# Optimization experiments

Hardware: AMD Instinct MI355X
Metric: run time of the kernel (lower is better)

Reference implementation:

```python
import jax, jax.numpy as jnp
import numpy as np
import math

VOCAB = 390
D = 512
D_INNER = 2048
H = 8
DH = D // H
L = 6
MAX_SEQ = 1024
BATCH = 4
OUT = 2
PAD = 0
EPS = 1e-6


def sinusoid(max_seq, d):
    pos = np.arange(max_seq, dtype=np.float64)[:, None]
    i = np.arange(d, dtype=np.float64)[None, :]
    angle = (pos * np.exp(-np.log(10000.0) * i / d) * np.exp(np.log(10000.0) / d * (i % 2))
             + 0.5 * np.pi * (i % 2))
    return np.sin(angle)[None].astype(np.float32)  # [1, max_seq, d]


def setup_inputs() -> dict:
    key = jax.random.key(0)
    ks = jax.random.split(key, 16)
    s = 0.02
    emb = jax.random.uniform(ks[0], (VOCAB, D), jnp.float32, -0.1, 0.1)
    emb = emb.at[PAD].set(0.0)  # padding_idx row zeroed
    inp = {
        'x': jax.random.randint(ks[1], (BATCH, MAX_SEQ), 0, VOCAB, dtype=jnp.int64) if jax.config.jax_enable_x64 else jax.random.randint(ks[1], (BATCH, MAX_SEQ), 0, VOCAB, dtype=jnp.int32),
        'emb': emb,
        'pos': jnp.asarray(sinusoid(MAX_SEQ, D)),
        'Wq': jax.random.normal(ks[2], (L, D, D), jnp.float32) * s,
        'bq': jnp.zeros((L, D), jnp.float32),
        'Wk': jax.random.normal(ks[3], (L, D, D), jnp.float32) * s,
        'bk': jnp.zeros((L, D), jnp.float32),
        'Wv': jax.random.normal(ks[4], (L, D, D), jnp.float32) * s,
        'bv': jnp.zeros((L, D), jnp.float32),
        'Wo': jax.random.normal(ks[5], (L, D, D), jnp.float32) * s,
        'bo': jnp.zeros((L, D), jnp.float32),
        'E': jax.random.normal(ks[6], (L, MAX_SEQ, DH), jnp.float32),
        'W1': jax.random.normal(ks[7], (L, D, D_INNER), jnp.float32) * s,
        'b1': jnp.zeros((L, D_INNER), jnp.float32),
        'W2': jax.random.normal(ks[8], (L, D_INNER, D), jnp.float32) * s,
        'b2': jnp.zeros((L, D), jnp.float32),
        'ln1_s': jnp.ones((L, D), jnp.float32),
        'ln1_b': jnp.zeros((L, D), jnp.float32),
        'ln2_s': jnp.ones((L, D), jnp.float32),
        'ln2_b': jnp.zeros((L, D), jnp.float32),
        'Wf': jax.random.normal(ks[9], (D, OUT), jnp.float32) * s,
        'bf': jnp.zeros((OUT,), jnp.float32),
    }
    return inp


def _layernorm(x, scale, bias):
    mu = jnp.mean(x, axis=-1, keepdims=True)
    var = jnp.mean(jnp.square(x - mu), axis=-1, keepdims=True)
    return (x - mu) * jax.lax.rsqrt(var + EPS) * scale + bias


def _rel_attention(x, Wq, bq, Wk, bk, Wv, bv, Wo, bo, E):
    b, s, d = x.shape
    q = (x @ Wq + bq).reshape(b, s, H, DH).transpose(0, 2, 1, 3)  # [b,h,s,dh]
    k = (x @ Wk + bk).reshape(b, s, H, DH).transpose(0, 2, 1, 3)
    v = (x @ Wv + bv).reshape(b, s, H, DH).transpose(0, 2, 1, 3)
    m = MAX_SEQ  # len_q == len_k == max_seq -> full E
    QE = jnp.einsum('bhld,md->bhlm', q, E)  # [b,h,s,m]
    # qe masking: keep position j >= m-1-i for query row i
    keep = (jnp.arange(m)[None, :] >= (m - 1 - jnp.arange(s))[:, None]).astype(QE.dtype)
    QE = QE * keep
    # skewing trick: pad-left on last dim, reshape, drop first row
    padded = jnp.pad(QE, ((0, 0), (0, 0), (0, 0), (1, 0)))  # [b,h,s,m+1]
    Srel = padded.reshape(b, H, m + 1, s)[:, :, 1:, :]  # [b,h,m,s] == [b,h,s,s]
    logits = (jnp.einsum('bhqd,bhkd->bhqk', q, k) + Srel) / math.sqrt(DH)
    attn = jax.nn.softmax(logits, axis=-1)
    out = jnp.einsum('bhqk,bhkd->bhqd', attn, v)
    out = out.transpose(0, 2, 1, 3).reshape(b, s, d)
    return out @ Wo + bo


def reference(x, emb, pos, Wq, bq, Wk, bk, Wv, bv, Wo, bo, E, W1, b1, W2, b2,
              ln1_s, ln1_b, ln2_s, ln2_b, Wf, bf):
    h = emb[x] * math.sqrt(D)  # [b,s,d]
    h = h + pos[:, :h.shape[1], :]
    for i in range(L):
        attn = _rel_attention(h, Wq[i], bq[i], Wk[i], bk[i], Wv[i], bv[i], Wo[i], bo[i], E[i])
        h1 = _layernorm(attn + h, ln1_s[i], ln1_b[i])
        ffn = jax.nn.relu(h1 @ W1[i] + b1[i]) @ W2[i] + b2[i]
        h = _layernorm(h1 + ffn, ln2_s[i], ln2_b[i])
    return jnp.tanh(h[:, 0, :] @ Wf + bf)  # [b, OUT]
```

## Files before the change

kernel.cpp:

```cpp
#include <hip/hip_runtime.h>
#include <math.h>

#define BATCH  4
#define SEQ    1024
#define DM     512
#define DI     2048
#define NH     8
#define DH     64
#define NL     6
#define NOUT   2

typedef unsigned short u16;
typedef short s16x8 __attribute__((ext_vector_type(8)));
typedef float f32x4 __attribute__((ext_vector_type(4)));
typedef unsigned short u16x4 __attribute__((ext_vector_type(4)));

#define MFMA16(a, b, c) __builtin_amdgcn_mfma_f32_16x16x32_bf16((a), (b), (c), 0, 0, 0)

static constexpr float SQRT_D = 22.627416997969522f;

#define SLOT_WO   786432
#define SLOT_W1   1048576
#define SLOT_W2   2097152
#define SLOT_E    3145728
#define SLOT_SZ   3211264

__device__ __forceinline__ u16 f2b(float x) {
    union { float f; unsigned u; } v; v.f = x;
    unsigned r = v.u + 0x7fffu + ((v.u >> 16) & 1u);
    return (u16)(r >> 16);
}
__device__ __forceinline__ float b2f(u16 b) {
    union { unsigned u; float f; } v; v.u = ((unsigned)b) << 16; return v.f;
}

__global__ __launch_bounds__(256) void k_embed(const int* __restrict__ x,
                                               const float* __restrict__ emb,
                                               const float* __restrict__ pos,
                                               float* __restrict__ h,
                                               u16* __restrict__ hb) {
    const int idx = blockIdx.x * 256 + threadIdx.x;
    const int d4  = idx & 127;
    const int bs  = idx >> 7;
    const int s   = bs & (SEQ - 1);
    const int tok = x[bs];
    const float4 e = ((const float4*)emb)[tok * 128 + d4];
    const float4 p = ((const float4*)pos)[s * 128 + d4];
    float4 r;
    r.x = e.x * SQRT_D + p.x;  r.y = e.y * SQRT_D + p.y;
    r.z = e.z * SQRT_D + p.z;  r.w = e.w * SQRT_D + p.w;
    ((float4*)h)[idx] = r;
    u16x4 rb = { f2b(r.x), f2b(r.y), f2b(r.z), f2b(r.w) };
    ((u16x4*)hb)[idx] = rb;
}

__global__ __launch_bounds__(256) void k_conv(const float* __restrict__ Wq, const float* __restrict__ Wk,
                                              const float* __restrict__ Wv, const float* __restrict__ Wo,
                                              const float* __restrict__ W1, const float* __restrict__ W2,
                                              const float* __restrict__ E,
                                              u16* __restrict__ wbase, int layer0, int slot_stride) {
    const int ll = blockIdx.x / 3136;
    const int tb = blockIdx.x - ll * 3136;
    const int layer = layer0 + ll;
    u16* Wqkvt = wbase + (size_t)ll * slot_stride;
    u16* Wot   = Wqkvt + SLOT_WO;
    u16* W1t   = Wqkvt + SLOT_W1;
    u16* W2t   = Wqkvt + SLOT_W2;
    u16* Ebf   = Wqkvt + SLOT_E;

    if (tb >= 3072) {
        const int rem = tb - 3072;
        const int idx = rem * 1024 + threadIdx.x * 4;
        const float4 v = *(const float4*)(E + (size_t)layer * SEQ * DH + idx);
        u16x4 o = { f2b(v.x), f2b(v.y), f2b(v.z), f2b(v.w) };
        *(u16x4*)(Ebf + idx) = o;
        return;
    }
    __shared__ float T[32][33];
    const float* src; u16* dst; int Ksz, Nsz, tk, tn;
    if (tb < 768) {
        const int mat = tb >> 8, rem = tb & 255;
        src = (mat == 0 ? Wq : (mat == 1 ? Wk : Wv)) + (size_t)layer * DM * DM;
        dst = Wqkvt + (size_t)mat * DM * DM;
        Ksz = 512; Nsz = 512; tk = rem & 15; tn = rem >> 4;
    } else if (tb < 1024) {
        const int rem = tb - 768;
        src = Wo + (size_t)layer * DM * DM; dst = Wot;
        Ksz = 512; Nsz = 512; tk = rem & 15; tn = rem >> 4;
    } else if (tb < 2048) {
        const int rem = tb - 1024;
        src = W1 + (size_t)layer * DM * DI; dst = W1t;
        Ksz = 512; Nsz = 2048; tk = rem & 15; tn = rem >> 4;
    } else {
        const int rem = tb - 2048;
        src = W2 + (size_t)layer * DI * DM; dst = W2t;
        Ksz = 2048; Nsz = 512; tk = rem >> 4; tn = rem & 15;
    }
    {
        const int rr = threadIdx.x >> 3, c4 = (threadIdx.x & 7) << 2;
        const float4 v = *(const float4*)(src + (size_t)(tk * 32 + rr) * Nsz + tn * 32 + c4);
        T[rr][c4 + 0] = v.x; T[rr][c4 + 1] = v.y; T[rr][c4 + 2] = v.z; T[rr][c4 + 3] = v.w;
    }
    __syncthreads();
    {
        const int nl = threadIdx.x >> 3, k4 = (threadIdx.x & 7) << 2;
        u16x4 o = { f2b(T[k4 + 0][nl]), f2b(T[k4 + 1][nl]), f2b(T[k4 + 2][nl]), f2b(T[k4 + 3][nl]) };
        *(u16x4*)(dst + (size_t)(tn * 32 + nl) * Ksz + tk * 32 + k4) = o;
    }
}

__global__ __launch_bounds__(256) void k_vt(const u16* __restrict__ vb,
                                            u16* __restrict__ Vt) {
    __shared__ float T[32][33];
    const int tn = blockIdx.x;
    const int tk = blockIdx.y;
    const int b  = blockIdx.z;
    const u16* src = vb + (size_t)b * SEQ * DM;
    u16* dst = Vt + (size_t)b * DM * SEQ;
    {
        const int rr = threadIdx.x >> 3, c4 = (threadIdx.x & 7) << 2;
        const u16x4 v = *(const u16x4*)(src + (size_t)(tk * 32 + rr) * DM + tn * 32 + c4);
        T[rr][c4 + 0] = b2f(v.x); T[rr][c4 + 1] = b2f(v.y);
        T[rr][c4 + 2] = b2f(v.z); T[rr][c4 + 3] = b2f(v.w);
    }
    __syncthreads();
    {
        const int nl = threadIdx.x >> 3, k4 = (threadIdx.x & 7) << 2;
        u16x4 o = { f2b(T[k4 + 0][nl]), f2b(T[k4 + 1][nl]),
                    f2b(T[k4 + 2][nl]), f2b(T[k4 + 3][nl]) };
        *(u16x4*)(dst + (size_t)(tn * 32 + nl) * SEQ + tk * 32 + k4) = o;
    }
}

template <int RELU, int WRITE_BF16>
__global__ __launch_bounds__(256) void k_mm(const u16* __restrict__ A,
                                            const u16* __restrict__ Bt,
                                            const float* __restrict__ bias0,
                                            const float* __restrict__ bias1,
                                            const float* __restrict__ bias2,
                                            float* __restrict__ Cf,
                                            u16* __restrict__ Cb,
                                            int K, int ldc, int seg_shift, size_t seg_stride) {
    __shared__ u16 As[128 * 40];
    __shared__ u16 Bs[128 * 40];

    const int n0 = blockIdx.x << 7;
    const int m0 = blockIdx.y << 7;
    const int t  = threadIdx.x;
    const int lane = t & 63, w = t >> 6;
    const int n16 = lane & 15, quad = lane >> 4;
    const int wr = (w & 1) << 6;
    const int wc = (w >> 1) << 6;

    const f32x4 z = {0.f, 0.f, 0.f, 0.f};
    f32x4 acc[4][4];
#pragma unroll
    for (int i = 0; i < 4; ++i)
#pragma unroll
        for (int j = 0; j < 4; ++j) acc[i][j] = z;

    const int sr = t >> 2, sk = (t & 3) << 3;
    const u16* Ag = A  + (size_t)(m0 + sr) * K + sk;
    const u16* Bg = Bt + (size_t)(n0 + sr) * K + sk;

    for (int k0 = 0; k0 < K; k0 += 32) {
        __syncthreads();
        *(uint4*)&As[sr * 40 + sk]        = *(const uint4*)(Ag + k0);
        *(uint4*)&As[(sr + 64) * 40 + sk] = *(const uint4*)(Ag + (size_t)64 * K + k0);
        *(uint4*)&Bs[sr * 40 + sk]        = *(const uint4*)(Bg + k0);
        *(uint4*)&Bs[(sr + 64) * 40 + sk] = *(const uint4*)(Bg + (size_t)64 * K + k0);
        __syncthreads();

        s16x8 af[4], bfr[4];
#pragma unroll
        for (int rb = 0; rb < 4; ++rb)
            af[rb] = *(const s16x8*)&As[(wr + rb * 16 + n16) * 40 + quad * 8];
#pragma unroll
        for (int cb = 0; cb < 4; ++cb)
            bfr[cb] = *(const s16x8*)&Bs[(wc + cb * 16 + n16) * 40 + quad * 8];
#pragma unroll
        for (int rb = 0; rb < 4; ++rb)
#pragma unroll
            for (int cb = 0; cb < 4; ++cb)
                acc[rb][cb] = MFMA16(af[rb], bfr[cb], acc[rb][cb]);
    }

    const int sel = n0 >> seg_shift;
    const int colbase = (n0 & ((1 << seg_shift) - 1)) + wc;
    const float* bias = (sel == 0) ? bias0 : (sel == 1 ? bias1 : bias2);
    const size_t cbase = (size_t)sel * seg_stride;

#pragma unroll
    for (int cb = 0; cb < 4; ++cb) {
        const int col = colbase + cb * 16 + n16;
        const float bv = bias[col];
#pragma unroll
        for (int rb = 0; rb < 4; ++rb) {
#pragma unroll
            for (int rr = 0; rr < 4; ++rr) {
                const int row = m0 + wr + rb * 16 + quad * 4 + rr;
                float v = acc[rb][cb][rr] + bv;
                if (RELU) v = fmaxf(v, 0.f);
                const size_t idx = cbase + (size_t)row * ldc + col;
                if (WRITE_BF16) Cb[idx] = f2b(v);
                else            Cf[idx] = v;
            }
        }
    }
}

__global__ __launch_bounds__(256) void k_attn(const u16* __restrict__ Qg,
                                              const u16* __restrict__ Kg,
                                              const u16* __restrict__ Vt,
                                              const u16* __restrict__ Eg,
                                              u16* __restrict__ Og) {
    __shared__ u16 Ks[64 * 72];
    __shared__ u16 Vts[64 * 72];
    __shared__ u16 Ps[64 * 72];
    __shared__ u16 Es[128 * 72];
    __shared__ float arena[64 * 130];

    const int i0 = blockIdx.x << 6;
    const int hd = blockIdx.y;
    const int b  = blockIdx.z;
    const int t  = threadIdx.x;
    const int lane = t & 63;
    const int n16 = lane & 15;
    const int quad = lane >> 4;
    const int rw = (t >> 6) << 4;
    const int ir_base = rw + (quad << 2);

    const size_t gb  = (size_t)b * SEQ * DM + hd * DH;
    const size_t vtb = ((size_t)b * DM + hd * DH) * SEQ;

    const u16* qp = Qg + gb + (size_t)(i0 + rw + n16) * DM + quad * 8;
    const s16x8 qa0 = *(const s16x8*)qp;
    const s16x8 qa1 = *(const s16x8*)(qp + 32);

    const f32x4 z = {0.f, 0.f, 0.f, 0.f};
    f32x4 Oa[4] = {z, z, z, z};
    float l_run[4] = {0.f, 0.f, 0.f, 0.f};

    for (int ct = 0; ct < 16; ++ct) {
        const int c0 = ct << 6;
        const bool active = (c0 <= i0);

        __syncthreads();
        {
            int c = t, r = c >> 3, k8 = (c & 7) << 3;
            *(uint4*)&Ks[r * 72 + k8] = *(const uint4*)(Kg + gb + (size_t)(c0 + r) * DM + k8);
            c = t + 256; r = c >> 3; k8 = (c & 7) << 3;
            *(uint4*)&Ks[r * 72 + k8] = *(const uint4*)(Kg + gb + (size_t)(c0 + r) * DM + k8);
        }
        {
            int c = t, d = c >> 3, j8 = (c & 7) << 3;
            *(uint4*)&Vts[d * 72 + j8] = *(const uint4*)(Vt + vtb + (size_t)d * SEQ + c0 + j8);
            c = t + 256; d = c >> 3; j8 = (c & 7) << 3;
            *(uint4*)&Vts[d * 72 + j8] = *(const uint4*)(Vt + vtb + (size_t)d * SEQ + c0 + j8);
        }
        if (active) {
            const int eb = 960 - i0 + c0;
#pragma unroll
            for (int p = 0; p < 4; ++p) {
                const int c = t + (p << 8);
                const int u = c >> 3, k8 = (c & 7) << 3;
                int m = eb + u; m = m > 1023 ? 1023 : m;
                *(uint4*)&Es[u * 72 + k8] = *(const uint4*)(Eg + (size_t)m * DH + k8);
            }
        }
        __syncthreads();

        f32x4 S[4];
#pragma unroll
        for (int cb = 0; cb < 4; ++cb) {
            const s16x8 k0 = *(const s16x8*)&Ks[(cb * 16 + n16) * 72 + quad * 8];
            const s16x8 k1 = *(const s16x8*)&Ks[(cb * 16 + n16) * 72 + quad * 8 + 32];
            S[cb] = MFMA16(qa0, k0, z);
            S[cb] = MFMA16(qa1, k1, S[cb]);
        }

        if (active) {
#pragma unroll
            for (int ub = 0; ub < 8; ++ub) {
                const s16x8 e0 = *(const s16x8*)&Es[(ub * 16 + n16) * 72 + quad * 8];
                const s16x8 e1 = *(const s16x8*)&Es[(ub * 16 + n16) * 72 + quad * 8 + 32];
                f32x4 qe = MFMA16(qa0, e0, z);
                qe = MFMA16(qa1, e1, qe);
#pragma unroll
                for (int rr = 0; rr < 4; ++rr)
                    arena[(ir_base + rr) * 130 + ub * 16 + n16] = qe[rr];
            }
            const int dqc = i0 - c0;
#pragma unroll
            for (int cb = 0; cb < 4; ++cb)
#pragma unroll
                for (int rr = 0; rr < 4; ++rr) {
                    const int ir = ir_base + rr;
                    const int d = cb * 16 + n16 - ir;
                    const float srel = (d <= dqc) ? arena[ir * 130 + 63 + d] : 0.f;
                    S[cb][rr] = (S[cb][rr] + srel) * 0.125f;
                }
        } else {
#pragma unroll
            for (int cb = 0; cb < 4; ++cb)
#pragma unroll
                for (int rr = 0; rr < 4; ++rr) S[cb][rr] *= 0.125f;
        }

        float p[4][4];
#pragma unroll
        for (int cb = 0; cb < 4; ++cb)
#pragma unroll
            for (int rr = 0; rr < 4; ++rr) p[cb][rr] = __expf(S[cb][rr]);
#pragma unroll
        for (int rr = 0; rr < 4; ++rr) {
            float rs = p[0][rr] + p[1][rr] + p[2][rr] + p[3][rr];
            rs += __shfl_xor(rs, 1, 64);
            rs += __shfl_xor(rs, 2, 64);
            rs += __shfl_xor(rs, 4, 64);
            rs += __shfl_xor(rs, 8, 64);
            l_run[rr] += rs;
        }

#pragma unroll
        for (int cb = 0; cb < 4; ++cb)
#pragma unroll
            for (int rr = 0; rr < 4; ++rr)
                Ps[(ir_base + rr) * 72 + cb * 16 + n16] = f2b(p[cb][rr]);

        const s16x8 pa0 = *(const s16x8*)&Ps[(rw + n16) * 72 + quad * 8];
        const s16x8 pa1 = *(const s16x8*)&Ps[(rw + n16) * 72 + quad * 8 + 32];
#pragma unroll
        for (int db = 0; db < 4; ++db) {
            const s16x8 v0 = *(const s16x8*)&Vts[(db * 16 + n16) * 72 + quad * 8];
            const s16x8 v1 = *(const s16x8*)&Vts[(db * 16 + n16) * 72 + quad * 8 + 32];
            Oa[db] = MFMA16(pa0, v0, Oa[db]);
            Oa[db] = MFMA16(pa1, v1, Oa[db]);
        }
    }

#pragma unroll
    for (int rr = 0; rr < 4; ++rr) l_run[rr] = 1.f / l_run[rr];
#pragma unroll
    for (int db = 0; db < 4; ++db)
#pragma unroll
        for (int rr = 0; rr < 4; ++rr) {
            const int row = i0 + ir_base + rr;
            Og[gb + (size_t)row * DM + db * 16 + n16] = f2b(Oa[db][rr] * l_run[rr]);
        }
}

__global__ __launch_bounds__(256) void k_ln(const float* __restrict__ A,
                                            const float* __restrict__ R,
                                            const float* __restrict__ sc,
                                            const float* __restrict__ bi,
                                            float* __restrict__ Y,
                                            u16* __restrict__ Yb) {
    const int g = threadIdx.x >> 7;
    const int r = (blockIdx.x << 1) + g;
    const int t = threadIdx.x & 127;
    const int w = threadIdx.x >> 6;
    const float4 a = ((const float4*)(A + (size_t)r * DM))[t];
    const float4 b = ((const float4*)(R + (size_t)r * DM))[t];
    float4 v;
    v.x = a.x + b.x; v.y = a.y + b.y; v.z = a.z + b.z; v.w = a.w + b.w;

    float s = v.x + v.y + v.z + v.w;
#pragma unroll
    for (int o = 32; o > 0; o >>= 1) s += __shfl_down(s, o, 64);
    __shared__ float r1[4], r2[4];
    if ((threadIdx.x & 63) == 0) r1[w] = s;
    __syncthreads();
    const float mean = (r1[g << 1] + r1[(g << 1) + 1]) * (1.f / 512.f);

    float4 d;
    d.x = v.x - mean; d.y = v.y - mean; d.z = v.z - mean; d.w = v.w - mean;
    float q = d.x * d.x + d.y * d.y + d.z * d.z + d.w * d.w;
#pragma unroll
    for (int o = 32; o > 0; o >>= 1) q += __shfl_down(q, o, 64);
    if ((threadIdx.x & 63) == 0) r2[w] = q;
    __syncthreads();
    const float rsq = rsqrtf((r2[g << 1] + r2[(g << 1) + 1]) * (1.f / 512.f) + 1e-6f);

    const float4 s4 = ((const float4*)sc)[t];
    const float4 b4 = ((const float4*)bi)[t];
    float4 y;
    y.x = d.x * rsq * s4.x + b4.x;
    y.y = d.y * rsq * s4.y + b4.y;
    y.z = d.z * rsq * s4.z + b4.z;
    y.w = d.w * rsq * s4.w + b4.w;
    ((float4*)(Y + (size_t)r * DM))[t] = y;
    u16x4 yb = { f2b(y.x), f2b(y.y), f2b(y.z), f2b(y.w) };
    ((u16x4*)(Yb + (size_t)r * DM))[t] = yb;
}

__global__ __launch_bounds__(512) void k_head(const float* __restrict__ h,
                                              const float* __restrict__ Wf,
                                              const float* __restrict__ bf,
                                              float* __restrict__ out) {
    const int t = threadIdx.x;
    const int w = t >> 6, lane = t & 63;
    const int b = w >> 1, oo = w & 1;
    float s = 0.f;
    for (int d = lane; d < DM; d += 64)
        s += h[(size_t)b * SEQ * DM + d] * Wf[d * NOUT + oo];
#pragma unroll
    for (int o = 32; o > 0; o >>= 1) s += __shfl_down(s, o, 64);
    if (lane == 0) out[b * NOUT + oo] = tanhf(s + bf[oo]);
}

extern "C" void kernel_launch(void* const* d_in, const int* in_sizes, int n_in,
                              void* d_out, int out_size, void* d_ws, size_t ws_size,
                              hipStream_t stream) {
    const int*   x    = (const int*)d_in[0];
    const float* emb  = (const float*)d_in[1];
    const float* pos  = (const float*)d_in[2];
    const float* Wq   = (const float*)d_in[3];
    const float* bq   = (const float*)d_in[4];
    const float* Wk   = (const float*)d_in[5];
    const float* bk   = (const float*)d_in[6];
    const float* Wv   = (const float*)d_in[7];
    const float* bv   = (const float*)d_in[8];
    const float* Wo   = (const float*)d_in[9];
    const float* bo   = (const float*)d_in[10];
    const float* E    = (const float*)d_in[11];
    const float* W1   = (const float*)d_in[12];
    const float* b1   = (const float*)d_in[13];
    const float* W2   = (const float*)d_in[14];
    const float* b2   = (const float*)d_in[15];
    const float* ln1s = (const float*)d_in[16];
    const float* ln1b = (const float*)d_in[17];
    const float* ln2s = (const float*)d_in[18];
    const float* ln2b = (const float*)d_in[19];
    const float* Wf   = (const float*)d_in[20];
    const float* bfp  = (const float*)d_in[21];
    float* out = (float*)d_out;

    char* W = (char*)d_ws;
    float* h    = (float*)(W);
    float* h1   = (float*)(W + (8u  << 20));
    u16*   hb   = (u16*)  (W + (16u << 20));
    u16*   h1b  = (u16*)  (W + (20u << 20));
    u16*   Vt   = h1b;
    u16*   qb   = (u16*)  (W + (24u << 20));
    u16*   kb   = (u16*)  (W + (28u << 20));
    u16*   vb   = (u16*)  (W + (32u << 20));
    u16*   tb   = (u16*)  (W + (36u << 20));
    u16*   midb = qb;
    u16*   Wb   = (u16*)  (W + (40u << 20));

    const bool all = ws_size >= (size_t)80478208ull;

    const int M = BATCH * SEQ;
    const size_t SEG = (size_t)M * DM;

    k_embed<<<(BATCH * SEQ * DM / 4) / 256, 256, 0, stream>>>(x, emb, pos, h, hb);
    if (all)
        k_conv<<<6 * 3136, 256, 0, stream>>>(Wq, Wk, Wv, Wo, W1, W2, E, Wb, 0, SLOT_SZ);

    for (int l = 0; l < NL; ++l) {
        if (!all)
            k_conv<<<3136, 256, 0, stream>>>(Wq, Wk, Wv, Wo, W1, W2, E, Wb, l, 0);
        u16* wl   = Wb + (size_t)(all ? l : 0) * SLOT_SZ;
        u16* wqkv = wl;
        u16* wot  = wl + SLOT_WO;
        u16* w1t  = wl + SLOT_W1;
        u16* w2t  = wl + SLOT_W2;
        u16* ebf  = wl + SLOT_E;

        k_mm<0, 1><<<dim3(12, 32), 256, 0, stream>>>(hb, wqkv,
            bq + l * DM, bk + l * DM, bv + l * DM, nullptr, qb, 512, 512, 9, SEG);
        k_vt<<<dim3(16, 32, 4), 256, 0, stream>>>(vb, Vt);
        k_attn<<<dim3(16, 8, 4), 256, 0, stream>>>(qb, kb, Vt, ebf, tb);
        k_mm<0, 0><<<dim3(4, 32), 256, 0, stream>>>(tb, wot,
            bo + l * DM, bo + l * DM, bo + l * DM, h1, nullptr, 512, 512, 30, 0);
        k_ln<<<M / 2, 256, 0, stream>>>(h1, h, ln1s + l * DM, ln1b + l * DM, h1, h1b);
        k_mm<1, 1><<<dim3(16, 32), 256, 0, stream>>>(h1b, w1t,
            b1 + l * DI, b1 + l * DI, b1 + l * DI, nullptr, midb, 512, 2048, 30, 0);
        k_mm<0, 0><<<dim3(4, 32), 256, 0, stream>>>(midb, w2t,
            b2 + l * DM, b2 + l * DM, b2 + l * DM, h, nullptr, 2048, 512, 30, 0);
        k_ln<<<M / 2, 256, 0, stream>>>(h, h1, ln2s + l * DM, ln2b + l * DM, h, hb);
    }

    k_head<<<1, 512, 0, stream>>>(h, Wf, bfp, out);
}
```

Before: 1.137 ms.

## Split-K output GEMMs, smaller QKV tiles, and prefetch/incremental E in attention

The Wo and W2 GEMMs gain a split-K variant over blockIdx.z that writes two partial sums, and a new 3-input layernorm adds them, so the 128-block grids get more blocks. The QKV projection moves to a new 64x128-tile kernel with a K-step of 64, doubling its grid. The attention kernel prefetches the next K/V/E tiles into registers, reuses half of the relative-position window from the previous tile, and stores QE logits in bf16 in a ring buffer instead of fp32. The costs are extra partial-sum traffic and a workspace-size condition, plus some precision loss in the relative logits.

New measurement: 1.004 ms. 1.13x faster.

```diff
diff --git a/kernel.cpp b/kernel.cpp
--- a/kernel.cpp
+++ b/kernel.cpp
@@ -135,17 +135,17 @@
 template <int RELU, int WRITE_BF16>
 __global__ __launch_bounds__(256) void k_mm(const u16* __restrict__ A,
                                             const u16* __restrict__ Bt,
-                                            const float* __restrict__ bias0,
-                                            const float* __restrict__ bias1,
-                                            const float* __restrict__ bias2,
-                                            float* __restrict__ Cf,
+                                            const float* __restrict__ bias,
+                                            float* __restrict__ Cf0,
+                                            float* __restrict__ Cf1,
                                             u16* __restrict__ Cb,
-                                            int K, int ldc, int seg_shift, size_t seg_stride) {
+                                            int K, int Kslice, int ldc) {
     __shared__ u16 As[128 * 40];
     __shared__ u16 Bs[128 * 40];
 
     const int n0 = blockIdx.x << 7;
     const int m0 = blockIdx.y << 7;
+    const int zz = blockIdx.z;
     const int t  = threadIdx.x;
     const int lane = t & 63, w = t >> 6;
     const int n16 = lane & 15, quad = lane >> 4;
@@ -160,10 +160,11 @@
         for (int j = 0; j < 4; ++j) acc[i][j] = z;
 
     const int sr = t >> 2, sk = (t & 3) << 3;
-    const u16* Ag = A  + (size_t)(m0 + sr) * K + sk;
-    const u16* Bg = Bt + (size_t)(n0 + sr) * K + sk;
-
-    for (int k0 = 0; k0 < K; k0 += 32) {
+    const int koff = zz * Kslice;
+    const u16* Ag = A  + (size_t)(m0 + sr) * K + koff + sk;
+    const u16* Bg = Bt + (size_t)(n0 + sr) * K + koff + sk;
+
+    for (int k0 = 0; k0 < Kslice; k0 += 32) {
         __syncthreads();
         *(uint4*)&As[sr * 40 + sk]        = *(const uint4*)(Ag + k0);
         *(uint4*)&As[(sr + 64) * 40 + sk] = *(const uint4*)(Ag + (size_t)64 * K + k0);
@@ -185,27 +186,94 @@
                 acc[rb][cb] = MFMA16(af[rb], bfr[cb], acc[rb][cb]);
     }
 
+    float* Cf = zz ? Cf1 : Cf0;
+#pragma unroll
+    for (int cb = 0; cb < 4; ++cb) {
+        const int col = n0 + wc + cb * 16 + n16;
+        const float bv = (zz == 0) ? bias[col] : 0.f;
+#pragma unroll
+        for (int rb = 0; rb < 4; ++rb) {
+#pragma unroll
+            for (int rr = 0; rr < 4; ++rr) {
+                const int row = m0 + wr + rb * 16 + quad * 4 + rr;
+                float v = acc[rb][cb][rr] + bv;
+                if (RELU) v = fmaxf(v, 0.f);
+                const size_t idx = (size_t)row * ldc + col;
+                if (WRITE_BF16) Cb[idx] = f2b(v);
+                else            Cf[idx] = v;
+            }
+        }
+    }
+}
+
+__global__ __launch_bounds__(256) void k_mm64(const u16* __restrict__ A,
+                                              const u16* __restrict__ Bt,
+                                              const float* __restrict__ bias0,
+                                              const float* __restrict__ bias1,
+                                              const float* __restrict__ bias2,
+                                              u16* __restrict__ Cb,
+                                              int K, int ldc, int seg_shift, size_t seg_stride) {
+    __shared__ u16 As[64 * 72];
+    __shared__ u16 Bs[128 * 72];
+
+    const int n0 = blockIdx.x << 7;
+    const int m0 = blockIdx.y << 6;
+    const int t  = threadIdx.x;
+    const int lane = t & 63, w = t >> 6;
+    const int n16 = lane & 15, quad = lane >> 4;
+    const int wc = w << 5;
+    const int r = t >> 3, o = (t & 7) << 3;
+
+    const f32x4 z = {0.f, 0.f, 0.f, 0.f};
+    f32x4 acc[4][2];
+#pragma unroll
+    for (int i = 0; i < 4; ++i) { acc[i][0] = z; acc[i][1] = z; }
+
+    const u16* Ag = A  + (size_t)(m0 + r) * K + o;
+    const u16* Bg = Bt + (size_t)(n0 + r) * K + o;
+
+    for (int k0 = 0; k0 < K; k0 += 64) {
+        __syncthreads();
+        *(uint4*)&As[r * 72 + o]        = *(const uint4*)(Ag + k0);
+        *(uint4*)&As[(r + 32) * 72 + o] = *(const uint4*)(Ag + (size_t)32 * K + k0);
+        *(uint4*)&Bs[r * 72 + o]        = *(const uint4*)(Bg + k0);
+        *(uint4*)&Bs[(r + 32) * 72 + o] = *(const uint4*)(Bg + (size_t)32 * K + k0);
+        *(uint4*)&Bs[(r + 64) * 72 + o] = *(const uint4*)(Bg + (size_t)64 * K + k0);
+        *(uint4*)&Bs[(r + 96) * 72 + o] = *(const uint4*)(Bg + (size_t)96 * K + k0);
+        __syncthreads();
+
+#pragma unroll
+        for (int ks = 0; ks < 2; ++ks) {
+            s16x8 af[4], bfr[2];
+#pragma unroll
+            for (int rb = 0; rb < 4; ++rb)
+                af[rb] = *(const s16x8*)&As[(rb * 16 + n16) * 72 + ks * 32 + quad * 8];
+#pragma unroll
+            for (int cb = 0; cb < 2; ++cb)
+                bfr[cb] = *(const s16x8*)&Bs[(wc + cb * 16 + n16) * 72 + ks * 32 + quad * 8];
+#pragma unroll
+            for (int rb = 0; rb < 4; ++rb)
+#pragma unroll
+                for (int cb = 0; cb < 2; ++cb)
+                    acc[rb][cb] = MFMA16(af[rb], bfr[cb], acc[rb][cb]);
+        }
+    }
+
     const int sel = n0 >> seg_shift;
     const int colbase = (n0 & ((1 << seg_shift) - 1)) + wc;
     const float* bias = (sel == 0) ? bias0 : (sel == 1 ? bias1 : bias2);
     const size_t cbase = (size_t)sel * seg_stride;
-
-#pragma unroll
-    for (int cb = 0; cb < 4; ++cb) {
+#pragma unroll
+    for (int cb = 0; cb < 2; ++cb) {
         const int col = colbase + cb * 16 + n16;
         const float bv = bias[col];
 #pragma unroll
-        for (int rb = 0; rb < 4; ++rb) {
+        for (int rb = 0; rb < 4; ++rb)
 #pragma unroll
             for (int rr = 0; rr < 4; ++rr) {
-                const int row = m0 + wr + rb * 16 + quad * 4 + rr;
-                float v = acc[rb][cb][rr] + bv;
-                if (RELU) v = fmaxf(v, 0.f);
-                const size_t idx = cbase + (size_t)row * ldc + col;
-                if (WRITE_BF16) Cb[idx] = f2b(v);
-                else            Cf[idx] = v;
+                const int row = m0 + rb * 16 + quad * 4 + rr;
+                Cb[cbase + (size_t)row * ldc + col] = f2b(acc[rb][cb][rr] + bv);
             }
-        }
     }
 }
 
@@ -218,7 +286,7 @@
     __shared__ u16 Vts[64 * 72];
     __shared__ u16 Ps[64 * 72];
     __shared__ u16 Es[128 * 72];
-    __shared__ float arena[64 * 130];
+    __shared__ u16 arena[128 * 72];
 
     const int i0 = blockIdx.x << 6;
     const int hd = blockIdx.y;
@@ -229,43 +297,67 @@
     const int quad = lane >> 4;
     const int rw = (t >> 6) << 4;
     const int ir_base = rw + (quad << 2);
+    const int a_last = i0 >> 6;
+    const int eb0 = 960 - i0;
 
     const size_t gb  = (size_t)b * SEQ * DM + hd * DH;
     const size_t vtb = ((size_t)b * DM + hd * DH) * SEQ;
+
+    const int r = t >> 3;
+    const int o = (t & 7) << 3;
 
     const u16* qp = Qg + gb + (size_t)(i0 + rw + n16) * DM + quad * 8;
     const s16x8 qa0 = *(const s16x8*)qp;
     const s16x8 qa1 = *(const s16x8*)(qp + 32);
 
+    uint4 kr0 = *(const uint4*)(Kg + gb + (size_t)r * DM + o);
+    uint4 kr1 = *(const uint4*)(Kg + gb + (size_t)(r + 32) * DM + o);
+    uint4 vr0 = *(const uint4*)(Vt + vtb + (size_t)r * SEQ + o);
+    uint4 vr1 = *(const uint4*)(Vt + vtb + (size_t)(r + 32) * SEQ + o);
+    int e0i = eb0 + r;        e0i = e0i > 1023 ? 1023 : e0i;
+    int e1i = eb0 + r + 32;   e1i = e1i > 1023 ? 1023 : e1i;
+    int e2i = eb0 + r + 64;   e2i = e2i > 1023 ? 1023 : e2i;
+    int e3i = eb0 + r + 96;   e3i = e3i > 1023 ? 1023 : e3i;
+    uint4 er0 = *(const uint4*)(Eg + (size_t)e0i * DH + o);
+    uint4 er1 = *(const uint4*)(Eg + (size_t)e1i * DH + o);
+    uint4 er2 = *(const uint4*)(Eg + (size_t)e2i * DH + o);
+    uint4 er3 = *(const uint4*)(Eg + (size_t)e3i * DH + o);
+
     const f32x4 z = {0.f, 0.f, 0.f, 0.f};
     f32x4 Oa[4] = {z, z, z, z};
     float l_run[4] = {0.f, 0.f, 0.f, 0.f};
 
     for (int ct = 0; ct < 16; ++ct) {
         const int c0 = ct << 6;
-        const bool active = (c0 <= i0);
+        const bool active = (ct <= a_last);
 
         __syncthreads();
-        {
-            int c = t, r = c >> 3, k8 = (c & 7) << 3;
-            *(uint4*)&Ks[r * 72 + k8] = *(const uint4*)(Kg + gb + (size_t)(c0 + r) * DM + k8);
-            c = t + 256; r = c >> 3; k8 = (c & 7) << 3;
-            *(uint4*)&Ks[r * 72 + k8] = *(const uint4*)(Kg + gb + (size_t)(c0 + r) * DM + k8);
-        }
-        {
-            int c = t, d = c >> 3, j8 = (c & 7) << 3;
-            *(uint4*)&Vts[d * 72 + j8] = *(const uint4*)(Vt + vtb + (size_t)d * SEQ + c0 + j8);
-            c = t + 256; d = c >> 3; j8 = (c & 7) << 3;
-            *(uint4*)&Vts[d * 72 + j8] = *(const uint4*)(Vt + vtb + (size_t)d * SEQ + c0 + j8);
-        }
-        if (active) {
-            const int eb = 960 - i0 + c0;
-#pragma unroll
-            for (int p = 0; p < 4; ++p) {
-                const int c = t + (p << 8);
-                const int u = c >> 3, k8 = (c & 7) << 3;
-                int m = eb + u; m = m > 1023 ? 1023 : m;
-                *(uint4*)&Es[u * 72 + k8] = *(const uint4*)(Eg + (size_t)m * DH + k8);
+        *(uint4*)&Ks[r * 72 + o]         = kr0;
+        *(uint4*)&Ks[(r + 32) * 72 + o]  = kr1;
+        *(uint4*)&Vts[r * 72 + o]        = vr0;
+        *(uint4*)&Vts[(r + 32) * 72 + o] = vr1;
+        if (ct == 0) {
+            *(uint4*)&Es[r * 72 + o]        = er0;
+            *(uint4*)&Es[(r + 32) * 72 + o] = er1;
+            *(uint4*)&Es[(r + 64) * 72 + o] = er2;
+            *(uint4*)&Es[(r + 96) * 72 + o] = er3;
+        } else if (active) {
+            const int nb = ((ct + 1) & 1) << 6;
+            *(uint4*)&Es[(nb + r) * 72 + o]      = er0;
+            *(uint4*)&Es[(nb + r + 32) * 72 + o] = er1;
+        }
+        if (ct < 15) {
+            const int cn = c0 + 64;
+            kr0 = *(const uint4*)(Kg + gb + (size_t)(cn + r) * DM + o);
+            kr1 = *(const uint4*)(Kg + gb + (size_t)(cn + r + 32) * DM + o);
+            vr0 = *(const uint4*)(Vt + vtb + (size_t)r * SEQ + cn + o);
+            vr1 = *(const uint4*)(Vt + vtb + (size_t)(r + 32) * SEQ + cn + o);
+            if (ct + 1 <= a_last) {
+                const int ebn = eb0 + 64 * (ct + 1) + 64;
+                int f0 = ebn + r;      f0 = f0 > 1023 ? 1023 : f0;
+                int f1 = ebn + r + 32; f1 = f1 > 1023 ? 1023 : f1;
+                er0 = *(const uint4*)(Eg + (size_t)f0 * DH + o);
+                er1 = *(const uint4*)(Eg + (size_t)f1 * DH + o);
             }
         }
         __syncthreads();
@@ -280,24 +372,38 @@
         }
 
         if (active) {
-#pragma unroll
-            for (int ub = 0; ub < 8; ++ub) {
-                const s16x8 e0 = *(const s16x8*)&Es[(ub * 16 + n16) * 72 + quad * 8];
-                const s16x8 e1 = *(const s16x8*)&Es[(ub * 16 + n16) * 72 + quad * 8 + 32];
-                f32x4 qe = MFMA16(qa0, e0, z);
-                qe = MFMA16(qa1, e1, qe);
-#pragma unroll
-                for (int rr = 0; rr < 4; ++rr)
-                    arena[(ir_base + rr) * 130 + ub * 16 + n16] = qe[rr];
+            if (ct == 0) {
+#pragma unroll
+                for (int ub = 0; ub < 8; ++ub) {
+                    const s16x8 e0 = *(const s16x8*)&Es[(ub * 16 + n16) * 72 + quad * 8];
+                    const s16x8 e1 = *(const s16x8*)&Es[(ub * 16 + n16) * 72 + quad * 8 + 32];
+                    f32x4 qe = MFMA16(qa0, e0, z);
+                    qe = MFMA16(qa1, e1, qe);
+                    u16x4 pk = { f2b(qe[0]), f2b(qe[1]), f2b(qe[2]), f2b(qe[3]) };
+                    *(u16x4*)&arena[(ub * 16 + n16) * 72 + ir_base] = pk;
+                }
+            } else {
+                const int pb = ((ct + 1) & 1) << 6;
+#pragma unroll
+                for (int ub = 0; ub < 4; ++ub) {
+                    const s16x8 e0 = *(const s16x8*)&Es[(pb + ub * 16 + n16) * 72 + quad * 8];
+                    const s16x8 e1 = *(const s16x8*)&Es[(pb + ub * 16 + n16) * 72 + quad * 8 + 32];
+                    f32x4 qe = MFMA16(qa0, e0, z);
+                    qe = MFMA16(qa1, e1, qe);
+                    u16x4 pk = { f2b(qe[0]), f2b(qe[1]), f2b(qe[2]), f2b(qe[3]) };
+                    *(u16x4*)&arena[(pb + ub * 16 + n16) * 72 + ir_base] = pk;
+                }
             }
             const int dqc = i0 - c0;
+            const int rot = ct << 6;
 #pragma unroll
             for (int cb = 0; cb < 4; ++cb)
 #pragma unroll
                 for (int rr = 0; rr < 4; ++rr) {
                     const int ir = ir_base + rr;
                     const int d = cb * 16 + n16 - ir;
-                    const float srel = (d <= dqc) ? arena[ir * 130 + 63 + d] : 0.f;
+                    const float srel = (d <= dqc)
+                        ? b2f(arena[((63 + d + rot) & 127) * 72 + ir]) : 0.f;
                     S[cb][rr] = (S[cb][rr] + srel) * 0.125f;
                 }
         } else {
@@ -364,6 +470,53 @@
     const float4 b = ((const float4*)(R + (size_t)r * DM))[t];
     float4 v;
     v.x = a.x + b.x; v.y = a.y + b.y; v.z = a.z + b.z; v.w = a.w + b.w;
+
+    float s = v.x + v.y + v.z + v.w;
+#pragma unroll
+    for (int o = 32; o > 0; o >>= 1) s += __shfl_down(s, o, 64);
+    __shared__ float r1[4], r2[4];
+    if ((threadIdx.x & 63) == 0) r1[w] = s;
+    __syncthreads();
+    const float mean = (r1[g << 1] + r1[(g << 1) + 1]) * (1.f / 512.f);
+
+    float4 d;
+    d.x = v.x - mean; d.y = v.y - mean; d.z = v.z - mean; d.w = v.w - mean;
+    float q = d.x * d.x + d.y * d.y + d.z * d.z + d.w * d.w;
+#pragma unroll
+    for (int o = 32; o > 0; o >>= 1) q += __shfl_down(q, o, 64);
+    if ((threadIdx.x & 63) == 0) r2[w] = q;
+    __syncthreads();
+    const float rsq = rsqrtf((r2[g << 1] + r2[(g << 1) + 1]) * (1.f / 512.f) + 1e-6f);
+
+    const float4 s4 = ((const float4*)sc)[t];
+    const float4 b4 = ((const float4*)bi)[t];
+    float4 y;
+    y.x = d.x * rsq * s4.x + b4.x;
+    y.y = d.y * rsq * s4.y + b4.y;
+    y.z = d.z * rsq * s4.z + b4.z;
+    y.w = d.w * rsq * s4.w + b4.w;
+    ((float4*)(Y + (size_t)r * DM))[t] = y;
+    u16x4 yb = { f2b(y.x), f2b(y.y), f2b(y.z), f2b(y.w) };
+    ((u16x4*)(Yb + (size_t)r * DM))[t] = yb;
+}
+
+__global__ __launch_bounds__(256) void k_ln3(const float* __restrict__ A0,
+                                             const float* __restrict__ A1,
+                                             const float* __restrict__ R,
+                                             const float* __restrict__ sc,
+                                             const float* __restrict__ bi,
+                                             float* __restrict__ Y,
+                                             u16* __restrict__ Yb) {
+    const int g = threadIdx.x >> 7;
+    const int r = (blockIdx.x << 1) + g;
+    const int t = threadIdx.x & 127;
+    const int w = threadIdx.x >> 6;
+    const float4 a0 = ((const float4*)(A0 + (size_t)r * DM))[t];
+    const float4 a1 = ((const float4*)(A1 + (size_t)r * DM))[t];
+    const float4 b  = ((const float4*)(R  + (size_t)r * DM))[t];
+    float4 v;
+    v.x = a0.x + a1.x + b.x; v.y = a0.y + a1.y + b.y;
+    v.z = a0.z + a1.z + b.z; v.w = a0.w + a1.w + b.w;
 
     float s = v.x + v.y + v.z + v.w;
 #pragma unroll
@@ -447,9 +600,13 @@
     u16*   vb   = (u16*)  (W + (32u << 20));
     u16*   tb   = (u16*)  (W + (36u << 20));
     u16*   midb = qb;
+    float* P1   = (float*)(W + (24u << 20));
     u16*   Wb   = (u16*)  (W + (40u << 20));
 
     const bool all = ws_size >= (size_t)80478208ull;
+    const size_t off_p2 = (40ull << 20) + (size_t)(all ? 6 : 1) * SLOT_SZ * 2;
+    const bool splitF2 = ws_size >= off_p2 + (8ull << 20);
+    float* P2 = (float*)(W + off_p2);
 
     const int M = BATCH * SEQ;
     const size_t SEG = (size_t)M * DM;
@@ -468,18 +625,24 @@
         u16* w2t  = wl + SLOT_W2;
         u16* ebf  = wl + SLOT_E;
 
-        k_mm<0, 1><<<dim3(12, 32), 256, 0, stream>>>(hb, wqkv,
-            bq + l * DM, bk + l * DM, bv + l * DM, nullptr, qb, 512, 512, 9, SEG);
+        k_mm64<<<dim3(12, 64), 256, 0, stream>>>(hb, wqkv,
+            bq + l * DM, bk + l * DM, bv + l * DM, qb, 512, 512, 9, SEG);
         k_vt<<<dim3(16, 32, 4), 256, 0, stream>>>(vb, Vt);
         k_attn<<<dim3(16, 8, 4), 256, 0, stream>>>(qb, kb, Vt, ebf, tb);
-        k_mm<0, 0><<<dim3(4, 32), 256, 0, stream>>>(tb, wot,
-            bo + l * DM, bo + l * DM, bo + l * DM, h1, nullptr, 512, 512, 30, 0);
-        k_ln<<<M / 2, 256, 0, stream>>>(h1, h, ln1s + l * DM, ln1b + l * DM, h1, h1b);
-        k_mm<1, 1><<<dim3(16, 32), 256, 0, stream>>>(h1b, w1t,
-            b1 + l * DI, b1 + l * DI, b1 + l * DI, nullptr, midb, 512, 2048, 30, 0);
-        k_mm<0, 0><<<dim3(4, 32), 256, 0, stream>>>(midb, w2t,
-            b2 + l * DM, b2 + l * DM, b2 + l * DM, h, nullptr, 2048, 512, 30, 0);
-        k_ln<<<M / 2, 256, 0, stream>>>(h, h1, ln2s + l * DM, ln2b + l * DM, h, hb);
+        k_mm<0, 0><<<dim3(4, 32, 2), 256, 0, stream>>>(tb, wot,
+            bo + l * DM, h1, P1, nullptr, 512, 256, 512);
+        k_ln3<<<M / 2, 256, 0, stream>>>(h1, P1, h, ln1s + l * DM, ln1b + l * DM, h1, h1b);
+        k_mm<1, 1><<<dim3(16, 32, 1), 256, 0, stream>>>(h1b, w1t,
+            b1 + l * DI, nullptr, nullptr, midb, 512, 512, 2048);
+        if (splitF2) {
+            k_mm<0, 0><<<dim3(4, 32, 2), 256, 0, stream>>>(midb, w2t,
+                b2 + l * DM, h, P2, nullptr, 2048, 1024, 512);
+            k_ln3<<<M / 2, 256, 0, stream>>>(h, P2, h1, ln2s + l * DM, ln2b + l * DM, h, hb);
+        } else {
+            k_mm<0, 0><<<dim3(4, 32, 1), 256, 0, stream>>>(midb, w2t,
+                b2 + l * DM, h, nullptr, nullptr, 2048, 2048, 512);
+            k_ln<<<M / 2, 256, 0, stream>>>(h, h1, ln2s + l * DM, ln2b + l * DM, h, hb);
+        }
     }
 
     k_head<<<1, 512, 0, stream>>>(h, Wf, bfp, out);
```
